# Optimization experiments

Measured on AMD Instinct MI355X. Metric: run time of the kernel, lower is better.

## Reference

```python
import jax, jax.numpy as jnp
import numpy as np

NUM_LABELS = 512
NUM_DEMOG = 4
N = 65536
D = 512


def setup_inputs() -> dict:
    key = jax.random.key(0)
    k1, k2, k3 = jax.random.split(key, 3)
    feats = jax.random.normal(k1, (N, D), dtype=jnp.float32)
    labels = jax.random.randint(k2, (N,), 0, NUM_LABELS, dtype=jnp.int64)
    demog_labels = jax.random.randint(k3, (N,), 0, NUM_DEMOG, dtype=jnp.int64)
    return {"feats": feats, "labels": labels, "demog_labels": demog_labels}


def reference(feats, labels, demog_labels):
    # Group id = (demog, label) pair -> flat segment id.
    G = NUM_DEMOG * NUM_LABELS
    seg = (demog_labels * NUM_LABELS + labels).astype(jnp.int32)  # [N]

    ones = jnp.ones((feats.shape[0],), dtype=feats.dtype)
    cnt = jax.ops.segment_sum(ones, seg, num_segments=G)          # [G]
    sums = jax.ops.segment_sum(feats, seg, num_segments=G)        # [G, D]
    safe_cnt = jnp.maximum(cnt, 1.0)
    mu = sums / safe_cnt[:, None]                                 # per-group mean

    # Per-sample squared distance to its group mean (== diagonal of the
    # centered Gram matrix in the original, without the O(n^2) matmul).
    d = feats - mu[seg]                                           # [N, D]
    sq = jnp.sum(d * d, axis=1)                                   # [N]

    grp_mean_dist = jax.ops.segment_sum(sq, seg, num_segments=G) / safe_cnt  # [G]

    present = (cnt > 0).astype(feats.dtype).reshape(NUM_DEMOG, NUM_LABELS)
    gm = grp_mean_dist.reshape(NUM_DEMOG, NUM_LABELS)
    # Mean over present (demog, subject) groups within each demog.
    intra = jnp.sum(gm * present, axis=1) / jnp.maximum(jnp.sum(present, axis=1), 1.0)  # [NUM_DEMOG]

    mu_intra = jnp.mean(intra)
    loss = jnp.mean(jnp.abs(intra - mu_intra))
    return loss
```

## Files before the change

### kernel.cpp

```cpp
#include <hip/hip_runtime.h>
#include <hip/hip_bf16.h>

#define NN 65536
#define DD 512
#define NUM_LABELS 512
#define NUM_DEMOG 4
#define GG (NUM_DEMOG * NUM_LABELS)
#define CAP 128
#define NSLICE 4

__global__ void k_hist(const int* __restrict__ labels,
                       const int* __restrict__ demog,
                       int* __restrict__ cnt,
                       int* __restrict__ order) {
    int i = blockIdx.x * blockDim.x + threadIdx.x;
    if (i >= NN) return;
    int seg = demog[i] * NUM_LABELS + labels[i];
    int pos = atomicAdd(&cnt[seg], 1);
    if (pos < CAP) order[seg * CAP + pos] = i;
}

__global__ __launch_bounds__(256, 4)
void k_group(const float* __restrict__ feats,
             const int* __restrict__ cnt,
             const int* __restrict__ order,
             float* __restrict__ part) {
    int t    = threadIdx.x;
    int lane = t & 63;
    int task = blockIdx.x * 4 + (t >> 6);
    int g     = task >> 2;
    int slice = task & 3;
    int tcol  = lane & 31;
    int rp    = lane >> 5;

    int idx0 = order[g * CAP + lane];
    int idx1 = order[g * CAP + 64 + lane];
    int c = cnt[g];
    if (c > CAP) c = CAP;
    idx0 = (lane < c) ? idx0 : 0;
    idx1 = (64 + lane < c) ? idx1 : 0;

    const float4* fv = (const float4*)feats;
    int fcol = slice * 32 + tcol;

    float4 acc = make_float4(0.f, 0.f, 0.f, 0.f);
    float ssq = 0.f;

    {
        float4 v[16];
#pragma unroll
        for (int k = 0; k < 16; ++k) {
            int row = __shfl(idx0, rp + 2 * k);
            v[k] = fv[(size_t)row * (DD / 4) + fcol];
        }
#pragma unroll
        for (int k = 0; k < 16; ++k) {
            float w = (rp + 2 * k < c) ? 1.f : 0.f;
            acc.x += w * v[k].x; acc.y += w * v[k].y;
            acc.z += w * v[k].z; acc.w += w * v[k].w;
            ssq += w * (v[k].x * v[k].x + v[k].y * v[k].y +
                        v[k].z * v[k].z + v[k].w * v[k].w);
        }
    }
    if (c > 32) {
        float4 v[16];
#pragma unroll
        for (int k = 0; k < 16; ++k) {
            int row = __shfl(idx0, 32 + rp + 2 * k);
            v[k] = fv[(size_t)row * (DD / 4) + fcol];
        }
#pragma unroll
        for (int k = 0; k < 16; ++k) {
            float w = (32 + rp + 2 * k < c) ? 1.f : 0.f;
            acc.x += w * v[k].x; acc.y += w * v[k].y;
            acc.z += w * v[k].z; acc.w += w * v[k].w;
            ssq += w * (v[k].x * v[k].x + v[k].y * v[k].y +
                        v[k].z * v[k].z + v[k].w * v[k].w);
        }
        for (int j = 64 + rp; j < c; j += 2) {
            int row = __shfl(idx1, j - 64);
            float4 v = fv[(size_t)row * (DD / 4) + fcol];
            acc.x += v.x; acc.y += v.y; acc.z += v.z; acc.w += v.w;
            ssq += v.x * v.x + v.y * v.y + v.z * v.z + v.w * v.w;
        }
    }

    acc.x += __shfl(acc.x, lane ^ 32);
    acc.y += __shfl(acc.y, lane ^ 32);
    acc.z += __shfl(acc.z, lane ^ 32);
    acc.w += __shfl(acc.w, lane ^ 32);
    float n2p = acc.x * acc.x + acc.y * acc.y + acc.z * acc.z + acc.w * acc.w;

    for (int off = 32; off > 0; off >>= 1) {
        ssq += __shfl_down(ssq, off);
        n2p += __shfl_down(n2p, off);
    }
    if (lane == 0) {
        float val = 0.f;
        if (c > 0) val = ssq - 0.5f * n2p / (float)c;
        part[task] = val;
    }
}

__global__ __launch_bounds__(256)
void k_final(const int* __restrict__ cnt,
             const float* __restrict__ part,
             float* __restrict__ out) {
    int t = threadIdx.x;
    __shared__ float sred[8];
    __shared__ float intra[NUM_DEMOG];

    for (int d = 0; d < NUM_DEMOG; ++d) {
        float s = 0.f;
        float p = 0.f;
        for (int l = t; l < NUM_LABELS; l += 256) {
            int g = d * NUM_LABELS + l;
            int c = cnt[g];
            if (c > 0) {
                float q = part[4 * g] + part[4 * g + 1] +
                          part[4 * g + 2] + part[4 * g + 3];
                s += q / (float)c;
                p += 1.f;
            }
        }
        for (int off = 32; off > 0; off >>= 1) {
            s += __shfl_down(s, off);
            p += __shfl_down(p, off);
        }
        if ((t & 63) == 0) {
            int wid = t >> 6;
            sred[wid * 2]     = s;
            sred[wid * 2 + 1] = p;
        }
        __syncthreads();
        if (t == 0) {
            float S = sred[0] + sred[2] + sred[4] + sred[6];
            float P = sred[1] + sred[3] + sred[5] + sred[7];
            intra[d] = S / fmaxf(P, 1.f);
        }
        __syncthreads();
    }
    if (t == 0) {
        float m = 0.f;
        for (int d = 0; d < NUM_DEMOG; ++d) m += intra[d];
        m *= (1.f / NUM_DEMOG);
        float l = 0.f;
        for (int d = 0; d < NUM_DEMOG; ++d) l += fabsf(intra[d] - m);
        out[0] = l * (1.f / NUM_DEMOG);
    }
}

extern "C" void kernel_launch(void* const* d_in, const int* in_sizes, int n_in,
                              void* d_out, int out_size, void* d_ws, size_t ws_size,
                              hipStream_t stream) {
    const float* feats = (const float*)d_in[0];
    const int* labels  = (const int*)d_in[1];
    const int* demog   = (const int*)d_in[2];
    float* out = (float*)d_out;

    int*   cnt   = (int*)d_ws;
    float* part  = (float*)(cnt + GG);
    int*   order = (int*)(part + GG * NSLICE);

    hipMemsetAsync(d_ws, 0, GG * sizeof(int), stream);

    k_hist<<<NN / 256, 256, 0, stream>>>(labels, demog, cnt, order);
    k_group<<<GG * NSLICE / 4, 256, 0, stream>>>(feats, cnt, order, part);
    k_group<<<GG * NSLICE / 4, 256, 0, stream>>>(feats, cnt, order, part);
    k_final<<<1, 256, 0, stream>>>(cnt, part, out);
}
```

Measured before the change: 237.4 us.

## Drop redundant k_group launch and remap group work to two 64-column slices

```diff
diff --git a/kernel.cpp b/kernel.cpp
--- a/kernel.cpp
+++ b/kernel.cpp
@@ -7,7 +7,7 @@
 #define NUM_DEMOG 4
 #define GG (NUM_DEMOG * NUM_LABELS)
 #define CAP 128
-#define NSLICE 4
+#define NSLICE 2
 
 __global__ void k_hist(const int* __restrict__ labels,
                        const int* __restrict__ demog,
@@ -20,7 +20,25 @@
     if (pos < CAP) order[seg * CAP + pos] = i;
 }
 
-__global__ __launch_bounds__(256, 4)
+#define GBATCH16(BASE, IDXREG)                                                \
+    {                                                                         \
+        float4 v[16];                                                         \
+        _Pragma("unroll")                                                     \
+        for (int k = 0; k < 16; ++k) {                                        \
+            int row = __shfl(IDXREG, (BASE & 63) + k);                        \
+            v[k] = fv[(size_t)row * (DD / 4) + fcol];                         \
+        }                                                                     \
+        _Pragma("unroll")                                                     \
+        for (int k = 0; k < 16; ++k) {                                        \
+            float w = (BASE + k < c) ? 1.f : 0.f;                             \
+            acc.x += w * v[k].x; acc.y += w * v[k].y;                         \
+            acc.z += w * v[k].z; acc.w += w * v[k].w;                         \
+            ssq += w * (v[k].x * v[k].x + v[k].y * v[k].y +                   \
+                        v[k].z * v[k].z + v[k].w * v[k].w);                   \
+        }                                                                     \
+    }
+
+__global__ __launch_bounds__(256)
 void k_group(const float* __restrict__ feats,
              const int* __restrict__ cnt,
              const int* __restrict__ order,
@@ -28,10 +46,8 @@
     int t    = threadIdx.x;
     int lane = t & 63;
     int task = blockIdx.x * 4 + (t >> 6);
-    int g     = task >> 2;
-    int slice = task & 3;
-    int tcol  = lane & 31;
-    int rp    = lane >> 5;
+    int g = task >> 1;
+    int s = task & 1;
 
     int idx0 = order[g * CAP + lane];
     int idx1 = order[g * CAP + 64 + lane];
@@ -41,63 +57,30 @@
     idx1 = (64 + lane < c) ? idx1 : 0;
 
     const float4* fv = (const float4*)feats;
-    int fcol = slice * 32 + tcol;
+    int fcol = s * 64 + lane;
 
     float4 acc = make_float4(0.f, 0.f, 0.f, 0.f);
     float ssq = 0.f;
 
-    {
-        float4 v[16];
-#pragma unroll
-        for (int k = 0; k < 16; ++k) {
-            int row = __shfl(idx0, rp + 2 * k);
-            v[k] = fv[(size_t)row * (DD / 4) + fcol];
-        }
-#pragma unroll
-        for (int k = 0; k < 16; ++k) {
-            float w = (rp + 2 * k < c) ? 1.f : 0.f;
-            acc.x += w * v[k].x; acc.y += w * v[k].y;
-            acc.z += w * v[k].z; acc.w += w * v[k].w;
-            ssq += w * (v[k].x * v[k].x + v[k].y * v[k].y +
-                        v[k].z * v[k].z + v[k].w * v[k].w);
-        }
-    }
-    if (c > 32) {
-        float4 v[16];
-#pragma unroll
-        for (int k = 0; k < 16; ++k) {
-            int row = __shfl(idx0, 32 + rp + 2 * k);
-            v[k] = fv[(size_t)row * (DD / 4) + fcol];
-        }
-#pragma unroll
-        for (int k = 0; k < 16; ++k) {
-            float w = (32 + rp + 2 * k < c) ? 1.f : 0.f;
-            acc.x += w * v[k].x; acc.y += w * v[k].y;
-            acc.z += w * v[k].z; acc.w += w * v[k].w;
-            ssq += w * (v[k].x * v[k].x + v[k].y * v[k].y +
-                        v[k].z * v[k].z + v[k].w * v[k].w);
-        }
-        for (int j = 64 + rp; j < c; j += 2) {
-            int row = __shfl(idx1, j - 64);
-            float4 v = fv[(size_t)row * (DD / 4) + fcol];
-            acc.x += v.x; acc.y += v.y; acc.z += v.z; acc.w += v.w;
-            ssq += v.x * v.x + v.y * v.y + v.z * v.z + v.w * v.w;
-        }
+    GBATCH16(0, idx0)
+    if (c > 16) GBATCH16(16, idx0)
+    if (c > 32) GBATCH16(32, idx0)
+    if (c > 48) GBATCH16(48, idx0)
+    for (int j = 64; j < c; ++j) {
+        int row = __shfl(idx1, j - 64);
+        float4 v = fv[(size_t)row * (DD / 4) + fcol];
+        acc.x += v.x; acc.y += v.y; acc.z += v.z; acc.w += v.w;
+        ssq += v.x * v.x + v.y * v.y + v.z * v.z + v.w * v.w;
     }
 
-    acc.x += __shfl(acc.x, lane ^ 32);
-    acc.y += __shfl(acc.y, lane ^ 32);
-    acc.z += __shfl(acc.z, lane ^ 32);
-    acc.w += __shfl(acc.w, lane ^ 32);
     float n2p = acc.x * acc.x + acc.y * acc.y + acc.z * acc.z + acc.w * acc.w;
-
     for (int off = 32; off > 0; off >>= 1) {
         ssq += __shfl_down(ssq, off);
         n2p += __shfl_down(n2p, off);
     }
     if (lane == 0) {
         float val = 0.f;
-        if (c > 0) val = ssq - 0.5f * n2p / (float)c;
+        if (c > 0) val = ssq - n2p / (float)c;
         part[task] = val;
     }
 }
@@ -117,8 +100,7 @@
             int g = d * NUM_LABELS + l;
             int c = cnt[g];
             if (c > 0) {
-                float q = part[4 * g] + part[4 * g + 1] +
-                          part[4 * g + 2] + part[4 * g + 3];
+                float q = part[2 * g] + part[2 * g + 1];
                 s += q / (float)c;
                 p += 1.f;
             }
@@ -166,6 +148,5 @@
 
     k_hist<<<NN / 256, 256, 0, stream>>>(labels, demog, cnt, order);
     k_group<<<GG * NSLICE / 4, 256, 0, stream>>>(feats, cnt, order, part);
-    k_group<<<GG * NSLICE / 4, 256, 0, stream>>>(feats, cnt, order, part);
     k_final<<<1, 256, 0, stream>>>(cnt, part, out);
 }
```

New measurement: 214.4 us. -9.7%, faster.
